# Kernel optimization log

Measured on AMD Instinct MI355X. Metric: run time of the kernel, lower is better.

The kernel has to match this reference:

```python
import jax, jax.numpy as jnp
import numpy as np

A_DIM = 6
VBR = jnp.array([300.0, 750.0, 1200.0, 1850.0, 2850.0, 4300.0])
MAX_BR = 4300.0
BUF = 30000.0  # buffer_size fixed to 30000 each forward
N_STEPS = 6    # unrolled iterations in the source (cooked_bw[0]..cooked_bw[5])


def _conv_feat(x, w, b):
    # 1-channel valid Conv1d(kernel=4) + ReLU, flattened channel-major like torch .view
    L = x.shape[0]
    idx = jnp.arange(L - 3)[:, None] + jnp.arange(4)[None, :]
    win = x[idx]                                   # (L-3, 4)
    out = jax.nn.relu(win @ w[:, 0, :].T + b)      # (L-3, 128)
    return out.T.reshape(-1)                       # (128*(L-3),)


def setup_inputs() -> dict:
    key = jax.random.key(0)
    ks = jax.random.split(key, 12)
    s = 0.1
    return {
        "inp": jax.random.uniform(ks[0], (8, 8), jnp.float32) + 0.1,
        "conv_w": jax.random.normal(ks[1], (128, 1, 4), jnp.float32) * s,
        "conv_b": jax.random.normal(ks[2], (128,), jnp.float32) * s,
        "w0": jax.random.normal(ks[3], (128, 1), jnp.float32) * s,
        "b0": jax.random.normal(ks[4], (128,), jnp.float32) * s,
        "w1": jax.random.normal(ks[5], (128, 1), jnp.float32) * s,
        "b1": jax.random.normal(ks[6], (128,), jnp.float32) * s,
        "w2": jax.random.normal(ks[7], (128, 1), jnp.float32) * s,
        "b2": jax.random.normal(ks[8], (128,), jnp.float32) * s,
        "w3": jax.random.normal(ks[9], (128, 2048), jnp.float32) * 0.02,
        "b3": jax.random.normal(ks[10], (128,), jnp.float32) * s,
        "w4": jax.random.normal(ks[11], (6, 128), jnp.float32) * s,
        "b4": jnp.zeros((6,), jnp.float32),
    }


def reference(inp, conv_w, conv_b, w0, b0, w1, b1, w2, b2, w3, b3, w4, b4):
    state = inp[:6, :]          # (6, 8)
    bw = inp[6, :]              # cooked bandwidth trace
    vs = inp[7, 0]              # base video chunk size
    vcs = vs * jnp.array([1.0, 2.0, 4.0, 8.0, 16.0, 32.0])  # video_chunk_sizes

    def net(st):
        s0 = jax.nn.relu(st[0, -1] * w0[:, 0] + b0)
        s1 = jax.nn.relu(st[1, -1] * w1[:, 0] + b1)
        s2 = _conv_feat(st[2, :], conv_w, conv_b)          # 640
        s3 = _conv_feat(st[3, :], conv_w, conv_b)          # 640
        s4 = _conv_feat(st[4, :A_DIM], conv_w, conv_b)     # 384
        s5 = st[4, -1] * w2[:, 0] + b2                     # no relu (matches source)
        feat = jnp.concatenate([s0, s1, s2, s3, s4, s5])   # (2048,)
        h = jax.nn.relu(w3 @ feat + b3)
        return w4 @ h + b4                                 # (6,)

    for i in range(N_STEPS):
        logits = net(state)
        a = jnp.argmax(logits)
        state = jnp.roll(state, -1, axis=1)
        delay = vcs[a] / bw[i] - BUF
        state = state.at[0, -1].set(VBR[a] / MAX_BR)
        state = state.at[1, -1].set(BUF / 1000.0 / 10.0)
        state = state.at[2, -1].set(vcs[a] / delay / 1000.0)
        state = state.at[3, -1].set(delay / 1000.0 / 10.0)
        state = state.at[4, :A_DIM].set(vcs / 1e6)
        state = state.at[5, -1].set((7.0 - i) / 8.0)

    return net(state)
```

## Files before the change

kernel.cpp:

```cpp
#include <hip/hip_runtime.h>

#define NBLK 32
#define TPB  256
#define PSTRIDE64 64

__device__ __forceinline__ float relu_(float x) { return fmaxf(x, 0.f); }


__launch_bounds__(TPB, 1)
__global__ void actor_kernel(
    const float* __restrict__ inp,
    const float* __restrict__ conv_w, const float* __restrict__ conv_b,
    const float* __restrict__ w0, const float* __restrict__ b0,
    const float* __restrict__ w1, const float* __restrict__ b1,
    const float* __restrict__ w2, const float* __restrict__ b2,
    const float* __restrict__ w3, const float* __restrict__ b3,
    const float* __restrict__ w4, const float* __restrict__ b4,
    float* __restrict__ out, int* __restrict__ flags,
    float* __restrict__ partials)
{
    const int tid = threadIdx.x;
    const int b   = blockIdx.x;

    unsigned long long* pub = (unsigned long long*)partials;

    __shared__ __align__(16) float lw3[4 * 2048];
    __shared__ __align__(16) float lfeat[2048];
    __shared__ __align__(16) float lc2[512], lc3[512];
    __shared__ float lbase2[128], lbase3[128], ls5[128];
    __shared__ float ls0[6 * 128];
    __shared__ float ltmp[512];
    __shared__ __align__(16) float lcw[512];
    __shared__ float lcb[128];
    __shared__ float lw0v[128], lb0v[128], lw1v[128], lb1v[128];
    __shared__ float lw2v[128], lb2v[128], lb3v[128];
    __shared__ float lw4[768], lb4v[8];
    __shared__ float st2[8], st3[8], st4[8];
    __shared__ float sx[8];
    __shared__ float lbw[8];
    __shared__ float h_lds[4], hv_lds[4 * 8];
    __shared__ float red[48];
    __shared__ float sval[32 * 48];
    __shared__ int   sact[2];

    {
        const float4* g4 = (const float4*)(w3 + b * 4 * 2048);
        float4* l4 = (float4*)lw3;
        for (int idx = tid; idx < 2048; idx += TPB) l4[idx] = g4[idx];
    }
    for (int idx = tid; idx < 512; idx += TPB) lcw[idx] = conv_w[idx];
    if (tid < 128) {
        lcb[tid]  = conv_b[tid];
        lw0v[tid] = w0[tid]; lb0v[tid] = b0[tid];
        lw1v[tid] = w1[tid]; lb1v[tid] = b1[tid];
        lw2v[tid] = w2[tid]; lb2v[tid] = b2[tid];
        lb3v[tid] = b3[tid];
    }
    for (int idx = tid; idx < 768; idx += TPB) lw4[idx] = w4[idx];
    if (tid < 6) lb4v[tid] = b4[tid];
    if (tid < 8) {
        st2[tid] = inp[16 + tid];
        st3[tid] = inp[24 + tid];
        st4[tid] = inp[32 + tid];
        lbw[tid] = inp[48 + tid];
    }
    if (tid == 0) {
        sx[0] = inp[7];   sx[1] = inp[15];
        sx[2] = inp[39];  sx[3] = inp[32];
        sx[4] = inp[56];
    }
    __syncthreads();

    if (tid < 128) {
        const float vb[6] = {300.f, 750.f, 1200.f, 1850.f, 2850.f, 4300.f};
        #pragma unroll
        for (int v = 0; v < 6; ++v)
            ls0[v * 128 + tid] = relu_(vb[v] * (1.f / 4300.f) * lw0v[tid] + lb0v[tid]);
        ltmp[tid] = relu_(3.0f * lw1v[tid] + lb1v[tid]);
    }
    for (int m = tid; m < 384; m += TPB) {
        int c = m / 3, w = m - c * 3;
        float a = lcb[c];
        #pragma unroll
        for (int k = 0; k < 4; ++k)
            a += sx[4] * (float)(1 << (w + k)) * 1e-6f * lcw[c * 4 + k];
        ltmp[128 + m] = relu_(a);
    }
    __syncthreads();

    const int wv = tid >> 6, lane = tid & 63;
    const float* wr = lw3 + wv * 2048;
    const float bias3 = lb3v[b * 4 + wv];

    float hs0p[6], hs14p;
    #pragma unroll
    for (int v = 0; v < 6; ++v)
        hs0p[v] = wr[lane] * ls0[v * 128 + lane] + wr[64 + lane] * ls0[v * 128 + 64 + lane];
    hs14p = wr[128 + lane] * ltmp[lane] + wr[192 + lane] * ltmp[64 + lane];
    #pragma unroll
    for (int k = 0; k < 6; ++k) {
        int m = lane + 64 * k;
        hs14p += wr[1536 + m] * ltmp[128 + m];
    }

    const float VBRc[6] = {300.f, 750.f, 1200.f, 1850.f, 2850.f, 4300.f};

    int tb[6], te[6], myN = 0;
    #pragma unroll
    for (int r = 0; r < 6; ++r) {
        int idx = tid + 256 * r;
        if (idx < 1344) { tb[myN] = idx / 42; te[myN] = idx - 42 * (idx / 42); ++myN; }
    }

    float fcom_f = 0.f;
    float lb2s[2], lb3s[2], b4f2[2], b4f3[2];
    float cw2s[2], cw3s[2], w32s[2], w33s[2], w42s[2], w43s[2];

    for (int g = 0; g < 3; ++g) {
        const int i = 2 * g;

        if (tid < 128) {
            lfeat[tid]        = relu_(sx[0] * lw0v[tid] + lb0v[tid]);
            lfeat[1920 + tid] =        sx[2] * lw2v[tid] + lb2v[tid];
            lbase2[tid] = st2[5] * lcw[tid*4] + st2[6] * lcw[tid*4+1]
                        + st2[7] * lcw[tid*4+2] + lcb[tid];
            lbase3[tid] = st3[5] * lcw[tid*4] + st3[6] * lcw[tid*4+1]
                        + st3[7] * lcw[tid*4+2] + lcb[tid];
            ls5[tid] = sx[3] * lw2v[tid] + lb2v[tid];
        } else {
            int j = tid - 128;
            lfeat[128 + j] = relu_(sx[1] * lw1v[j] + lb1v[j]);
        }
        for (int m = tid; m < 640; m += TPB) {
            int c = m / 5, w = m - c * 5;
            float a2 = lcb[c], a3 = lcb[c];
            #pragma unroll
            for (int k = 0; k < 4; ++k) {
                float cw = lcw[c * 4 + k];
                a2 += st2[w + k] * cw;
                a3 += st3[w + k] * cw;
            }
            lfeat[256 + m] = relu_(a2);
            lfeat[896 + m] = relu_(a3);
        }
        for (int m = tid; m < 384; m += TPB) {
            int c = m / 3, w = m - c * 3;
            float a4 = lcb[c];
            #pragma unroll
            for (int k = 0; k < 4; ++k) a4 += st4[w + k] * lcw[c * 4 + k];
            lfeat[1536 + m] = relu_(a4);
        }
        for (int m = tid; m < 512; m += TPB) {
            int c = m >> 2, w = m & 3;
            float a2 = lcb[c], a3 = lcb[c];
            #pragma unroll
            for (int k = 0; k < 4; ++k) {
                float cw = lcw[c * 4 + k];
                a2 += st2[w + 1 + k] * cw;
                a3 += st3[w + 1 + k] * cw;
            }
            lc2[m] = relu_(a2);
            lc3[m] = relu_(a3);
        }
        __syncthreads();

        float acc_i;
        {
            const float4* w4p = (const float4*)wr;
            const float4* f4p = (const float4*)lfeat;
            float4 acc = make_float4(0.f, 0.f, 0.f, 0.f);
            #pragma unroll
            for (int it = 0; it < 8; ++it) {
                float4 a = w4p[it * 64 + lane];
                float4 f = f4p[it * 64 + lane];
                acc.x += a.x * f.x; acc.y += a.y * f.y;
                acc.z += a.z * f.z; acc.w += a.w * f.w;
            }
            acc_i = (acc.x + acc.y) + (acc.z + acc.w);
        }

        float s5c = wr[1920 + lane] * ls5[lane] + wr[1984 + lane] * ls5[64 + lane];
        float acc_c = hs14p + s5c;
        #pragma unroll
        for (int k = 0; k < 8; ++k) {
            int m = lane + 64 * k;
            int col = 256 + (m >> 2) * 5 + (m & 3);
            acc_c += wr[col] * lc2[m] + wr[640 + col] * lc3[m];
        }

        float n2[6], n3[6];
        {
            float bwi = lbw[i], vs = sx[4];
            #pragma unroll
            for (int v = 0; v < 6; ++v) {
                float vca   = vs * (float)(1 << v);
                float delay = vca / bwi - 30000.f;
                n2[v] = vca / delay * 1e-3f;
                n3[v] = delay * 1e-4f;
            }
        }
        float accv[6];
        #pragma unroll
        for (int v = 0; v < 6; ++v) accv[v] = hs0p[v];
        #pragma unroll
        for (int t = 0; t < 2; ++t) {
            int c = lane + 64 * t;
            float cw3 = lcw[c * 4 + 3];
            float bb2 = lbase2[c], bb3 = lbase3[c];
            float wc2 = wr[256 + c * 5 + 4], wc3 = wr[896 + c * 5 + 4];
            #pragma unroll
            for (int v = 0; v < 6; ++v)
                accv[v] += relu_(bb2 + n2[v] * cw3) * wc2
                         + relu_(bb3 + n3[v] * cw3) * wc3;
        }

        if (g == 2) {
            fcom_f = hs14p + s5c;
            #pragma unroll
            for (int t = 0; t < 2; ++t) {
                int c = lane + 64 * t;
                float c0 = lcw[c*4], c1 = lcw[c*4+1], c2 = lcw[c*4+2], c3 = lcw[c*4+3];
                cw2s[t] = c2; cw3s[t] = c3;
                lb2s[t] = lbase2[c];  lb3s[t] = lbase3[c];
                b4f2[t] = st2[6]*c0 + st2[7]*c1 + lcb[c];
                b4f3[t] = st3[6]*c0 + st3[7]*c1 + lcb[c];
                w32s[t] = wr[256 + c*5 + 3]; w33s[t] = wr[896 + c*5 + 3];
                w42s[t] = wr[256 + c*5 + 4]; w43s[t] = wr[896 + c*5 + 4];
                #pragma unroll
                for (int w = 0; w < 3; ++w) {
                    float a2 = st2[2+w]*c0 + st2[3+w]*c1 + st2[4+w]*c2 + st2[5+w]*c3 + lcb[c];
                    float a3 = st3[2+w]*c0 + st3[3+w]*c1 + st3[4+w]*c2 + st3[5+w]*c3 + lcb[c];
                    fcom_f += relu_(a2) * wr[256 + c*5 + w] + relu_(a3) * wr[896 + c*5 + w];
                }
            }
        }

        #pragma unroll
        for (int off = 32; off > 0; off >>= 1) {
            acc_i += __shfl_xor(acc_i, off);
            acc_c += __shfl_xor(acc_c, off);
            #pragma unroll
            for (int v = 0; v < 6; ++v) accv[v] += __shfl_xor(accv[v], off);
        }
        if (lane == 0) {
            h_lds[wv] = relu_(acc_i + bias3);
            #pragma unroll
            for (int v = 0; v < 6; ++v)
                hv_lds[wv * 8 + v] = relu_(acc_c + accv[v] + bias3);
        }
        __syncthreads();

        if (tid < 42) {
            int q = tid / 6, t = tid - q * 6;
            float p = 0.f;
            if (q == 0) {
                #pragma unroll
                for (int w = 0; w < 4; ++w) p += lw4[t * 128 + b * 4 + w] * h_lds[w];
            } else {
                #pragma unroll
                for (int w = 0; w < 4; ++w) p += lw4[t * 128 + b * 4 + w] * hv_lds[w * 8 + (q - 1)];
            }
            union { float f[2]; unsigned long long u; } x;
            x.f[0] = p; x.f[1] = (float)(g + 1);
            __hip_atomic_store(&pub[(g * NBLK + b) * PSTRIDE64 + tid], x.u,
                               __ATOMIC_RELAXED, __HIP_MEMORY_SCOPE_AGENT);
        }

        {
            const unsigned int seqbits = __float_as_uint((float)(g + 1));
            unsigned int pend = (1u << myN) - 1u;
            while (pend) {
                unsigned long long v[6];
                #pragma unroll
                for (int k = 0; k < 6; ++k) {
                    if (k < myN && (pend & (1u << k)))
                        v[k] = __hip_atomic_load(
                            &pub[(g * NBLK + tb[k]) * PSTRIDE64 + te[k]],
                            __ATOMIC_RELAXED, __HIP_MEMORY_SCOPE_AGENT);
                }
                #pragma unroll
                for (int k = 0; k < 6; ++k) {
                    if (k < myN && (pend & (1u << k))) {
                        if ((unsigned int)(v[k] >> 32) == seqbits) {
                            sval[tb[k] * 48 + te[k]] =
                                __uint_as_float((unsigned int)(v[k] & 0xFFFFFFFFu));
                            pend &= ~(1u << k);
                        }
                    }
                }
                if (pend) __builtin_amdgcn_s_sleep(1);
            }
        }
        __syncthreads();

        if (tid < 42) {
            float p = lb4v[tid % 6];
            #pragma unroll
            for (int bb = 0; bb < NBLK; ++bb) p += sval[bb * 48 + tid];
            red[tid] = p;
        }
        __syncthreads();
        if (tid == 0) {
            float best = red[0]; int a0 = 0;
            #pragma unroll
            for (int r = 1; r < 6; ++r) if (red[r] > best) { best = red[r]; a0 = r; }
            best = red[6 + 6 * a0]; int a1 = 0;
            #pragma unroll
            for (int r = 1; r < 6; ++r)
                if (red[6 + 6 * a0 + r] > best) { best = red[6 + 6 * a0 + r]; a1 = r; }

            if (g == 2) {
                sact[0] = a0; sact[1] = a1;
            } else {
                {
                    float vca = sx[4] * (float)(1 << a0);
                    float delay = vca / lbw[i] - 30000.f;
                    sx[0] = VBRc[a0] * (1.f / 4300.f);
                    sx[1] = 3.0f;
                    #pragma unroll
                    for (int c = 0; c < 7; ++c) { st2[c] = st2[c + 1]; st3[c] = st3[c + 1]; }
                    st2[7] = vca / delay * 1e-3f;
                    st3[7] = delay * 1e-4f;
                    sx[2] = sx[3]; sx[3] = sx[4] * 1e-6f;
                    #pragma unroll
                    for (int j = 0; j < 6; ++j) st4[j] = sx[4] * (float)(1 << j) * 1e-6f;
                }
                {
                    float vca = sx[4] * (float)(1 << a1);
                    float delay = vca / lbw[i + 1] - 30000.f;
                    sx[0] = VBRc[a1] * (1.f / 4300.f);
                    sx[1] = 3.0f;
                    #pragma unroll
                    for (int c = 0; c < 7; ++c) { st2[c] = st2[c + 1]; st3[c] = st3[c + 1]; }
                    st2[7] = vca / delay * 1e-3f;
                    st3[7] = delay * 1e-4f;
                    sx[2] = sx[3]; sx[3] = sx[4] * 1e-6f;
                    #pragma unroll
                    for (int j = 0; j < 6; ++j) st4[j] = sx[4] * (float)(1 << j) * 1e-6f;
                }
            }
        }
        __syncthreads();
    }

    {
        const int a4 = sact[0], a5 = sact[1];
        float vs = sx[4];
        float vca4 = vs * (float)(1 << a4);
        float d4   = vca4 / lbw[4] - 30000.f;
        float ap24 = vca4 / d4 * 1e-3f, ap34 = d4 * 1e-4f;
        float vca5 = vs * (float)(1 << a5);
        float d5   = vca5 / lbw[5] - 30000.f;
        float ap25 = vca5 / d5 * 1e-3f, ap35 = d5 * 1e-4f;

        float h0 = hs0p[0];
        h0 = (a5 == 1) ? hs0p[1] : h0;
        h0 = (a5 == 2) ? hs0p[2] : h0;
        h0 = (a5 == 3) ? hs0p[3] : h0;
        h0 = (a5 == 4) ? hs0p[4] : h0;
        h0 = (a5 == 5) ? hs0p[5] : h0;

        float hl = fcom_f + h0;
        #pragma unroll
        for (int t = 0; t < 2; ++t) {
            float r32 = relu_(lb2s[t] + ap24 * cw3s[t]);
            float r33 = relu_(lb3s[t] + ap34 * cw3s[t]);
            float r42 = relu_(b4f2[t] + ap24 * cw2s[t] + ap25 * cw3s[t]);
            float r43 = relu_(b4f3[t] + ap34 * cw2s[t] + ap35 * cw3s[t]);
            hl += r32 * w32s[t] + r33 * w33s[t] + r42 * w42s[t] + r43 * w43s[t];
        }
        #pragma unroll
        for (int off = 32; off > 0; off >>= 1) hl += __shfl_xor(hl, off);
        if (lane == 0) h_lds[wv] = relu_(hl + bias3);
    }
    __syncthreads();

    if (tid < 6) {
        float p = 0.f;
        #pragma unroll
        for (int w = 0; w < 4; ++w) p += lw4[tid * 128 + b * 4 + w] * h_lds[w];
        union { float f[2]; unsigned long long u; } x;
        x.f[0] = p; x.f[1] = 4.0f;
        __hip_atomic_store(&pub[(3 * NBLK + b) * PSTRIDE64 + tid], x.u,
                           __ATOMIC_RELAXED, __HIP_MEMORY_SCOPE_AGENT);
    }
    if (b == 0) {
        if (tid < 192) {
            int bb = tid / 6, e = tid - 6 * bb;
            const unsigned int seqbits = __float_as_uint(4.0f);
            for (;;) {
                unsigned long long u = __hip_atomic_load(
                    &pub[(3 * NBLK + bb) * PSTRIDE64 + e],
                    __ATOMIC_RELAXED, __HIP_MEMORY_SCOPE_AGENT);
                if ((unsigned int)(u >> 32) == seqbits) {
                    sval[bb * 48 + e] =
                        __uint_as_float((unsigned int)(u & 0xFFFFFFFFu));
                    break;
                }
                __builtin_amdgcn_s_sleep(1);
            }
        }
        __syncthreads();
        if (tid < 6) {
            float p = lb4v[tid];
            #pragma unroll
            for (int bb = 0; bb < NBLK; ++bb) p += sval[bb * 48 + tid];
            out[tid] = p;
        }
    }
}

extern "C" void kernel_launch(void* const* d_in, const int* in_sizes, int n_in,
                              void* d_out, int out_size, void* d_ws, size_t ws_size,
                              hipStream_t stream) {
    const float* inp    = (const float*)d_in[0];
    const float* conv_w = (const float*)d_in[1];
    const float* conv_b = (const float*)d_in[2];
    const float* w0     = (const float*)d_in[3];
    const float* b0     = (const float*)d_in[4];
    const float* w1     = (const float*)d_in[5];
    const float* b1     = (const float*)d_in[6];
    const float* w2     = (const float*)d_in[7];
    const float* b2     = (const float*)d_in[8];
    const float* w3     = (const float*)d_in[9];
    const float* b3     = (const float*)d_in[10];
    const float* w4     = (const float*)d_in[11];
    const float* b4     = (const float*)d_in[12];

    int*   flags    = (int*)d_ws;
    float* partials = (float*)((char*)d_ws + 8192);

    actor_kernel<<<NBLK, TPB, 0, stream>>>(inp, conv_w, conv_b,
                                           w0, b0, w1, b1, w2, b2,
                                           w3, b3, w4, b4,
                                           (float*)d_out, flags, partials);
}
```

Before: 98.95 us.

## Speculate all 36 final-step action pairs to remove last grid-wide sync round

```diff
diff --git a/kernel.cpp b/kernel.cpp
--- a/kernel.cpp
+++ b/kernel.cpp
@@ -3,6 +3,8 @@
 #define NBLK 32
 #define TPB  256
 #define PSTRIDE64 64
+#define R3BASE 4096
+#define R3STRIDE 320
 
 __device__ __forceinline__ float relu_(float x) { return fmaxf(x, 0.f); }
 
@@ -41,6 +43,9 @@
     __shared__ float h_lds[4], hv_lds[4 * 8];
     __shared__ float red[48];
     __shared__ float sval[32 * 48];
+    __shared__ float hscr[4 * 2368];
+    __shared__ float h36_lds[144];
+    __shared__ float sfan[258 * 32];
     __shared__ int   sact[2];
 
     {
@@ -111,10 +116,6 @@
         int idx = tid + 256 * r;
         if (idx < 1344) { tb[myN] = idx / 42; te[myN] = idx - 42 * (idx / 42); ++myN; }
     }
-
-    float fcom_f = 0.f;
-    float lb2s[2], lb3s[2], b4f2[2], b4f3[2];
-    float cw2s[2], cw3s[2], w32s[2], w33s[2], w42s[2], w43s[2];
 
     for (int g = 0; g < 3; ++g) {
         const int i = 2 * g;
@@ -215,7 +216,9 @@
         }
 
         if (g == 2) {
-            fcom_f = hs14p + s5c;
+            float fcom_f = hs14p + s5c;
+            float lb2s[2], lb3s[2], b4f2[2], b4f3[2];
+            float cw2s[2], cw3s[2], w32s[2], w33s[2], w42s[2], w43s[2];
             #pragma unroll
             for (int t = 0; t < 2; ++t) {
                 int c = lane + 64 * t;
@@ -233,6 +236,39 @@
                     fcom_f += relu_(a2) * wr[256 + c*5 + w] + relu_(a3) * wr[896 + c*5 + w];
                 }
             }
+            float ap5[6], ap35[6];
+            {
+                float bw5 = lbw[5], vs = sx[4];
+                #pragma unroll
+                for (int v = 0; v < 6; ++v) {
+                    float vca = vs * (float)(1 << v);
+                    float d   = vca / bw5 - 30000.f;
+                    ap5[v]  = vca / d * 1e-3f;
+                    ap35[v] = d * 1e-4f;
+                }
+            }
+            const int sbase = wv * 2368 + lane * 37;
+            #pragma unroll
+            for (int u = 0; u < 6; ++u) {
+                float r32[2], r33[2];
+                #pragma unroll
+                for (int t = 0; t < 2; ++t) {
+                    r32[t] = relu_(lb2s[t] + n2[u] * cw3s[t]);
+                    r33[t] = relu_(lb3s[t] + n3[u] * cw3s[t]);
+                }
+                #pragma unroll
+                for (int v = 0; v < 6; ++v) {
+                    float hl = fcom_f + hs0p[v];
+                    #pragma unroll
+                    for (int t = 0; t < 2; ++t) {
+                        float r42 = relu_(b4f2[t] + n2[u] * cw2s[t] + ap5[v]  * cw3s[t]);
+                        float r43 = relu_(b4f3[t] + n3[u] * cw2s[t] + ap35[v] * cw3s[t]);
+                        hl += r32[t] * w32s[t] + r33[t] * w33s[t]
+                            + r42 * w42s[t] + r43 * w43s[t];
+                    }
+                    hscr[sbase + u * 6 + v] = hl;
+                }
+            }
         }
 
         #pragma unroll
@@ -250,68 +286,66 @@
         }
         __syncthreads();
 
-        if (tid < 42) {
-            int q = tid / 6, t = tid - q * 6;
-            float p = 0.f;
-            if (q == 0) {
-                #pragma unroll
-                for (int w = 0; w < 4; ++w) p += lw4[t * 128 + b * 4 + w] * h_lds[w];
-            } else {
-                #pragma unroll
-                for (int w = 0; w < 4; ++w) p += lw4[t * 128 + b * 4 + w] * hv_lds[w * 8 + (q - 1)];
-            }
-            union { float f[2]; unsigned long long u; } x;
-            x.f[0] = p; x.f[1] = (float)(g + 1);
-            __hip_atomic_store(&pub[(g * NBLK + b) * PSTRIDE64 + tid], x.u,
-                               __ATOMIC_RELAXED, __HIP_MEMORY_SCOPE_AGENT);
-        }
-
-        {
-            const unsigned int seqbits = __float_as_uint((float)(g + 1));
-            unsigned int pend = (1u << myN) - 1u;
-            while (pend) {
-                unsigned long long v[6];
-                #pragma unroll
-                for (int k = 0; k < 6; ++k) {
-                    if (k < myN && (pend & (1u << k)))
-                        v[k] = __hip_atomic_load(
-                            &pub[(g * NBLK + tb[k]) * PSTRIDE64 + te[k]],
-                            __ATOMIC_RELAXED, __HIP_MEMORY_SCOPE_AGENT);
-                }
-                #pragma unroll
-                for (int k = 0; k < 6; ++k) {
-                    if (k < myN && (pend & (1u << k))) {
-                        if ((unsigned int)(v[k] >> 32) == seqbits) {
-                            sval[tb[k] * 48 + te[k]] =
-                                __uint_as_float((unsigned int)(v[k] & 0xFFFFFFFFu));
-                            pend &= ~(1u << k);
+        if (g < 2) {
+            if (tid < 42) {
+                int q = tid / 6, t = tid - q * 6;
+                float p = 0.f;
+                if (q == 0) {
+                    #pragma unroll
+                    for (int w = 0; w < 4; ++w) p += lw4[t * 128 + b * 4 + w] * h_lds[w];
+                } else {
+                    #pragma unroll
+                    for (int w = 0; w < 4; ++w) p += lw4[t * 128 + b * 4 + w] * hv_lds[w * 8 + (q - 1)];
+                }
+                union { float f[2]; unsigned long long u; } x;
+                x.f[0] = p; x.f[1] = (float)(g + 1);
+                __hip_atomic_store(&pub[(g * NBLK + b) * PSTRIDE64 + tid], x.u,
+                                   __ATOMIC_RELAXED, __HIP_MEMORY_SCOPE_AGENT);
+            }
+
+            {
+                const unsigned int seqbits = __float_as_uint((float)(g + 1));
+                unsigned int pend = (1u << myN) - 1u;
+                while (pend) {
+                    unsigned long long v[6];
+                    #pragma unroll
+                    for (int k = 0; k < 6; ++k) {
+                        if (k < myN && (pend & (1u << k)))
+                            v[k] = __hip_atomic_load(
+                                &pub[(g * NBLK + tb[k]) * PSTRIDE64 + te[k]],
+                                __ATOMIC_RELAXED, __HIP_MEMORY_SCOPE_AGENT);
+                    }
+                    #pragma unroll
+                    for (int k = 0; k < 6; ++k) {
+                        if (k < myN && (pend & (1u << k))) {
+                            if ((unsigned int)(v[k] >> 32) == seqbits) {
+                                sval[tb[k] * 48 + te[k]] =
+                                    __uint_as_float((unsigned int)(v[k] & 0xFFFFFFFFu));
+                                pend &= ~(1u << k);
+                            }
                         }
                     }
-                }
-                if (pend) __builtin_amdgcn_s_sleep(1);
-            }
-        }
-        __syncthreads();
-
-        if (tid < 42) {
-            float p = lb4v[tid % 6];
-            #pragma unroll
-            for (int bb = 0; bb < NBLK; ++bb) p += sval[bb * 48 + tid];
-            red[tid] = p;
-        }
-        __syncthreads();
-        if (tid == 0) {
-            float best = red[0]; int a0 = 0;
-            #pragma unroll
-            for (int r = 1; r < 6; ++r) if (red[r] > best) { best = red[r]; a0 = r; }
-            best = red[6 + 6 * a0]; int a1 = 0;
-            #pragma unroll
-            for (int r = 1; r < 6; ++r)
-                if (red[6 + 6 * a0 + r] > best) { best = red[6 + 6 * a0 + r]; a1 = r; }
-
-            if (g == 2) {
-                sact[0] = a0; sact[1] = a1;
-            } else {
+                    if (pend) __builtin_amdgcn_s_sleep(1);
+                }
+            }
+            __syncthreads();
+
+            if (tid < 42) {
+                float p = lb4v[tid % 6];
+                #pragma unroll
+                for (int bb = 0; bb < NBLK; ++bb) p += sval[bb * 48 + tid];
+                red[tid] = p;
+            }
+            __syncthreads();
+            if (tid == 0) {
+                float best = red[0]; int a0 = 0;
+                #pragma unroll
+                for (int r = 1; r < 6; ++r) if (red[r] > best) { best = red[r]; a0 = r; }
+                best = red[6 + 6 * a0]; int a1 = 0;
+                #pragma unroll
+                for (int r = 1; r < 6; ++r)
+                    if (red[6 + 6 * a0 + r] > best) { best = red[6 + 6 * a0 + r]; a1 = r; }
+
                 {
                     float vca = sx[4] * (float)(1 << a0);
                     float delay = vca / lbw[i] - 30000.f;
@@ -339,73 +373,104 @@
                     for (int j = 0; j < 6; ++j) st4[j] = sx[4] * (float)(1 << j) * 1e-6f;
                 }
             }
-        }
-        __syncthreads();
-    }
-
-    {
-        const int a4 = sact[0], a5 = sact[1];
-        float vs = sx[4];
-        float vca4 = vs * (float)(1 << a4);
-        float d4   = vca4 / lbw[4] - 30000.f;
-        float ap24 = vca4 / d4 * 1e-3f, ap34 = d4 * 1e-4f;
-        float vca5 = vs * (float)(1 << a5);
-        float d5   = vca5 / lbw[5] - 30000.f;
-        float ap25 = vca5 / d5 * 1e-3f, ap35 = d5 * 1e-4f;
-
-        float h0 = hs0p[0];
-        h0 = (a5 == 1) ? hs0p[1] : h0;
-        h0 = (a5 == 2) ? hs0p[2] : h0;
-        h0 = (a5 == 3) ? hs0p[3] : h0;
-        h0 = (a5 == 4) ? hs0p[4] : h0;
-        h0 = (a5 == 5) ? hs0p[5] : h0;
-
-        float hl = fcom_f + h0;
-        #pragma unroll
-        for (int t = 0; t < 2; ++t) {
-            float r32 = relu_(lb2s[t] + ap24 * cw3s[t]);
-            float r33 = relu_(lb3s[t] + ap34 * cw3s[t]);
-            float r42 = relu_(b4f2[t] + ap24 * cw2s[t] + ap25 * cw3s[t]);
-            float r43 = relu_(b4f3[t] + ap34 * cw2s[t] + ap35 * cw3s[t]);
-            hl += r32 * w32s[t] + r33 * w33s[t] + r42 * w42s[t] + r43 * w43s[t];
-        }
-        #pragma unroll
-        for (int off = 32; off > 0; off >>= 1) hl += __shfl_xor(hl, off);
-        if (lane == 0) h_lds[wv] = relu_(hl + bias3);
-    }
-    __syncthreads();
-
-    if (tid < 6) {
-        float p = 0.f;
-        #pragma unroll
-        for (int w = 0; w < 4; ++w) p += lw4[tid * 128 + b * 4 + w] * h_lds[w];
-        union { float f[2]; unsigned long long u; } x;
-        x.f[0] = p; x.f[1] = 4.0f;
-        __hip_atomic_store(&pub[(3 * NBLK + b) * PSTRIDE64 + tid], x.u,
-                           __ATOMIC_RELAXED, __HIP_MEMORY_SCOPE_AGENT);
-    }
-    if (b == 0) {
-        if (tid < 192) {
-            int bb = tid / 6, e = tid - 6 * bb;
-            const unsigned int seqbits = __float_as_uint(4.0f);
-            for (;;) {
-                unsigned long long u = __hip_atomic_load(
-                    &pub[(3 * NBLK + bb) * PSTRIDE64 + e],
-                    __ATOMIC_RELAXED, __HIP_MEMORY_SCOPE_AGENT);
-                if ((unsigned int)(u >> 32) == seqbits) {
-                    sval[bb * 48 + e] =
-                        __uint_as_float((unsigned int)(u & 0xFFFFFFFFu));
-                    break;
-                }
-                __builtin_amdgcn_s_sleep(1);
-            }
-        }
-        __syncthreads();
-        if (tid < 6) {
-            float p = lb4v[tid];
-            #pragma unroll
-            for (int bb = 0; bb < NBLK; ++bb) p += sval[bb * 48 + tid];
-            out[tid] = p;
+            __syncthreads();
+        } else {
+            if (tid < 144) {
+                const int wvr = tid / 36, m = tid - 36 * wvr;
+                const int base = wvr * 2368 + m;
+                float a[64];
+                #pragma unroll
+                for (int l = 0; l < 64; ++l) a[l] = hscr[base + l * 37];
+                #pragma unroll
+                for (int off = 32; off > 0; off >>= 1)
+                    #pragma unroll
+                    for (int ii = 0; ii < 32; ++ii)
+                        if (ii < off) a[ii] += a[ii + off];
+                h36_lds[wvr * 36 + m] = relu_(a[0] + lb3v[b * 4 + wvr]);
+            }
+            __syncthreads();
+
+            for (int e = tid; e < 258; e += TPB) {
+                float p = 0.f;
+                if (e < 42) {
+                    int q = e / 6, t = e - q * 6;
+                    if (q == 0) {
+                        #pragma unroll
+                        for (int w = 0; w < 4; ++w) p += lw4[t * 128 + b * 4 + w] * h_lds[w];
+                    } else {
+                        #pragma unroll
+                        for (int w = 0; w < 4; ++w) p += lw4[t * 128 + b * 4 + w] * hv_lds[w * 8 + (q - 1)];
+                    }
+                } else {
+                    int c = (e - 42) / 6, t = (e - 42) - 6 * ((e - 42) / 6);
+                    #pragma unroll
+                    for (int w = 0; w < 4; ++w) p += lw4[t * 128 + b * 4 + w] * h36_lds[w * 36 + c];
+                }
+                union { float f[2]; unsigned long long u; } x;
+                x.f[0] = p; x.f[1] = 3.0f;
+                __hip_atomic_store(&pub[R3BASE + b * R3STRIDE + e], x.u,
+                                   __ATOMIC_RELAXED, __HIP_MEMORY_SCOPE_AGENT);
+            }
+
+            if (b == 0) {
+                const unsigned int seqbits = __float_as_uint(3.0f);
+                const int nt = (tid < 64) ? 33 : 32;
+                unsigned long long pend = (nt == 33) ? ((1ull << 33) - 1ull)
+                                                     : ((1ull << 32) - 1ull);
+                while (pend) {
+                    unsigned long long v[33];
+                    #pragma unroll
+                    for (int r = 0; r < 33; ++r) {
+                        if (r < nt && (pend & (1ull << r))) {
+                            int idx = (r < 32) ? (tid + 256 * r) : (8192 + tid);
+                            int bb = idx / 258, e = idx - 258 * bb;
+                            v[r] = __hip_atomic_load(&pub[R3BASE + bb * R3STRIDE + e],
+                                                     __ATOMIC_RELAXED,
+                                                     __HIP_MEMORY_SCOPE_AGENT);
+                        }
+                    }
+                    #pragma unroll
+                    for (int r = 0; r < 33; ++r) {
+                        if (r < nt && (pend & (1ull << r))) {
+                            if ((unsigned int)(v[r] >> 32) == seqbits) {
+                                int idx = (r < 32) ? (tid + 256 * r) : (8192 + tid);
+                                int bb = idx / 258, e = idx - 258 * bb;
+                                sfan[e * 32 + bb] =
+                                    __uint_as_float((unsigned int)(v[r] & 0xFFFFFFFFu));
+                                pend &= ~(1ull << r);
+                            }
+                        }
+                    }
+                    if (pend) __builtin_amdgcn_s_sleep(1);
+                }
+                __syncthreads();
+
+                if (tid < 42) {
+                    float p = lb4v[tid % 6];
+                    #pragma unroll
+                    for (int bb = 0; bb < NBLK; ++bb) p += sfan[tid * 32 + bb];
+                    red[tid] = p;
+                }
+                __syncthreads();
+                if (tid == 0) {
+                    float best = red[0]; int a0 = 0;
+                    #pragma unroll
+                    for (int r = 1; r < 6; ++r) if (red[r] > best) { best = red[r]; a0 = r; }
+                    best = red[6 + 6 * a0]; int a1 = 0;
+                    #pragma unroll
+                    for (int r = 1; r < 6; ++r)
+                        if (red[6 + 6 * a0 + r] > best) { best = red[6 + 6 * a0 + r]; a1 = r; }
+                    sact[0] = a0; sact[1] = a1;
+                }
+                __syncthreads();
+                if (tid < 6) {
+                    float p = lb4v[tid];
+                    const int e = 42 + (sact[0] * 6 + sact[1]) * 6 + tid;
+                    #pragma unroll
+                    for (int bb = 0; bb < NBLK; ++bb) p += sfan[e * 32 + bb];
+                    out[tid] = p;
+                }
+            }
         }
     }
 }
```

After: 105.4 us. +6.6%, slower.
